# Kernel optimization log

Measured on AMD Instinct MI355X. Metric: run time of the kernel, lower is better.

Reference implementation:

```python
import jax, jax.numpy as jnp
import numpy as np

B, S, D = 2, 2048, 1024
H, HD = 16, 64          # n_heads, head_dim (H*HD == D)
E, K, F = 8, 2, 1024    # n_experts, top_k, expert hidden size
EPS = 1e-6


def setup_inputs() -> dict:
    key = jax.random.key(0)
    ks = jax.random.split(key, 10)
    g = lambda k, shape, sc: jax.random.normal(k, shape, jnp.float32) * sc
    return {
        "x": g(ks[0], (B, S, D), 1.0),
        "attn_norm_w": jnp.ones((D,), jnp.float32),
        "wq": g(ks[1], (D, D), 0.02),
        "wk": g(ks[2], (D, D), 0.02),
        "wv": g(ks[3], (D, D), 0.02),
        "wo": g(ks[4], (D, D), 0.02),
        "ffn_norm_w": jnp.ones((D,), jnp.float32),
        "router_w": g(ks[5], (D, E), 0.02),
        "w1": g(ks[6], (E, D, F), 0.02),  # gate proj per expert
        "w3": g(ks[7], (E, D, F), 0.02),  # up proj per expert
        "w2": g(ks[8], (E, F, D), 0.02),  # down proj per expert
    }


def rmsnorm(x, w):
    return x * jax.lax.rsqrt(jnp.mean(x * x, axis=-1, keepdims=True) + EPS) * w


def attention(x, wq, wk, wv, wo):
    b, s, d = x.shape
    q = (x @ wq).reshape(b, s, H, HD)
    k = (x @ wk).reshape(b, s, H, HD)
    v = (x @ wv).reshape(b, s, H, HD)
    scores = jnp.einsum("bqhd,bkhd->bhqk", q, k) / jnp.sqrt(jnp.float32(HD))
    causal = jnp.tril(jnp.ones((s, s), bool))
    scores = jnp.where(causal, scores, jnp.finfo(scores.dtype).min)
    p = jax.nn.softmax(scores, axis=-1)
    o = jnp.einsum("bhqk,bkhd->bqhd", p, v).reshape(b, s, d)
    return o @ wo


def moe_ffn(x, router_w, w1, w2, w3):
    b, s, d = x.shape
    xt = x.reshape(-1, d)                       # [T, D]
    probs = jax.nn.softmax(xt @ router_w, axis=-1)  # [T, E]
    gate, idx = jax.lax.top_k(probs, K)         # [T, K]
    gate = gate / jnp.sum(gate, axis=-1, keepdims=True)  # renormalize top-k
    T = xt.shape[0]
    combine = jnp.zeros((T, E), xt.dtype).at[jnp.arange(T)[:, None], idx].set(gate)
    out = jnp.zeros_like(xt)
    for e in range(E):  # fixed small loop over experts (dense-equivalent dispatch)
        h = jax.nn.silu(xt @ w1[e]) * (xt @ w3[e])
        out = out + combine[:, e:e + 1] * (h @ w2[e])
    return out.reshape(b, s, d)


def reference(x, attn_norm_w, wq, wk, wv, wo, ffn_norm_w, router_w, w1, w2, w3):
    # h = x + dropout(attn(norm(x)));  out = h + dropout(moe(norm(h)))  (dropout=0)
    h = x + attention(rmsnorm(x, attn_norm_w), wq, wk, wv, wo)
    return h + moe_ffn(rmsnorm(h, ffn_norm_w), router_w, w1, w2, w3)
```

## Files before the change

### kernel.cpp

```cpp
#include <hip/hip_runtime.h>
#include <cstdint>
#include <math.h>

typedef unsigned short u16;
typedef unsigned int u32;
typedef __bf16 bf16x8 __attribute__((ext_vector_type(8)));
typedef float f32x4 __attribute__((ext_vector_type(4)));

#define TBATCH 2
#define TSEQ   2048
#define TDIM   1024
#define THEADS 16
#define THDIM  64
#define TEXP   8
#define TFF    1024
#define TTOK   (TBATCH*TSEQ)
#define TPAIRS (TTOK*2)

__device__ __forceinline__ u16 f2bf(float f) {
  u32 u = __float_as_uint(f);
  u += 0x7FFFu + ((u >> 16) & 1u);
  return (u16)(u >> 16);
}
__device__ __forceinline__ u16 f2bft(float f) {
  return (u16)(__float_as_uint(f) >> 16);
}
__device__ __forceinline__ float bf2f(u16 h) { return __uint_as_float(((u32)h) << 16); }
__device__ __forceinline__ float fexp2(float x) {
  float r;
  asm("v_exp_f32 %0, %1" : "=v"(r) : "v"(x));
  return r;
}

__device__ __forceinline__ void gll16(const void* g, void* l) {
  __builtin_amdgcn_global_load_lds((const __attribute__((address_space(1))) void*)g,
                                   (__attribute__((address_space(3))) void*)l, 16, 0, 0);
}
__device__ __forceinline__ bf16x8 ldsread(const void* p) { return *(const bf16x8*)p; }
__device__ __forceinline__ f32x4 mm16(bf16x8 a, bf16x8 b, f32x4 c) {
  return __builtin_amdgcn_mfma_f32_16x16x32_bf16(a, b, c, 0, 0, 0);
}
__device__ __forceinline__ f32x4 fzero() { f32x4 z = {0.f, 0.f, 0.f, 0.f}; return z; }

__global__ void transpose_all_k(const float* __restrict__ wq, const float* __restrict__ wk,
                                const float* __restrict__ wv, const float* __restrict__ wo,
                                const float* __restrict__ w1, const float* __restrict__ w3,
                                const float* __restrict__ w2,
                                u16* __restrict__ qth, u16* __restrict__ qtl,
                                u16* __restrict__ kth, u16* __restrict__ ktl,
                                u16* __restrict__ vth_, u16* __restrict__ vtl_,
                                u16* __restrict__ oth, u16* __restrict__ otl,
                                u16* __restrict__ w1t, u16* __restrict__ w3t, u16* __restrict__ w2t) {
  __shared__ float t[32][33];
  int id = (int)blockIdx.x;
  const float* in; u16* outh; u16* outl = nullptr;
  size_t bo = 0;
  int tile;
  if (id < 4096) {
    const int wi = id >> 10;
    in   = (wi == 0) ? wq  : (wi == 1) ? wk  : (wi == 2) ? wv   : wo;
    outh = (wi == 0) ? qth : (wi == 1) ? kth : (wi == 2) ? vth_ : oth;
    outl = (wi == 0) ? qtl : (wi == 1) ? ktl : (wi == 2) ? vtl_ : otl;
    tile = id & 1023;
  } else {
    const int id2 = id - 4096;
    const int wi = id2 >> 13;
    const int rem = id2 & 8191;
    bo = (size_t)(rem >> 10) << 20;
    in   = (wi == 0) ? w1  : (wi == 1) ? w3  : w2;
    outh = (wi == 0) ? w1t : (wi == 1) ? w3t : w2t;
    tile = rem & 1023;
  }
  const int c0 = (tile & 31) * 32, r0 = (tile >> 5) * 32;
  const int tx = threadIdx.x, ty = threadIdx.y;
#pragma unroll
  for (int j = 0; j < 32; j += 8)
    t[ty + j][tx] = in[bo + (size_t)(r0 + ty + j) * 1024 + (c0 + tx)];
  __syncthreads();
#pragma unroll
  for (int j = 0; j < 32; j += 8) {
    float v = t[tx][ty + j];
    u16 hv = f2bf(v);
    size_t o = bo + (size_t)(c0 + ty + j) * 1024 + (r0 + tx);
    outh[o] = hv;
    if (outl != nullptr) outl[o] = f2bf(v - bf2f(hv));
  }
}

__launch_bounds__(256)
__global__ void rmsnorm_k(const float* __restrict__ x, const float* __restrict__ w,
                          u16* __restrict__ oh, u16* __restrict__ ol) {
  const int t = blockIdx.x, tid = threadIdx.x;
  const float4 xv = ((const float4*)(x + (size_t)t * TDIM))[tid];
  float ss = xv.x*xv.x + xv.y*xv.y + xv.z*xv.z + xv.w*xv.w;
#pragma unroll
  for (int d = 1; d < 64; d <<= 1) ss += __shfl_xor(ss, d, 64);
  __shared__ float sp[4];
  if ((tid & 63) == 0) sp[tid >> 6] = ss;
  __syncthreads();
  const float rsc = rsqrtf((sp[0] + sp[1] + sp[2] + sp[3]) * (1.0f / TDIM) + 1e-6f);
  const float4 wv = ((const float4*)w)[tid];
  float v0 = xv.x*rsc*wv.x, v1 = xv.y*rsc*wv.y, v2 = xv.z*rsc*wv.z, v3 = xv.w*rsc*wv.w;
  u16 h0 = f2bf(v0), h1 = f2bf(v1), h2 = f2bf(v2), h3 = f2bf(v3);
  uint2 ph; ph.x = (u32)h0 | ((u32)h1 << 16); ph.y = (u32)h2 | ((u32)h3 << 16);
  *(uint2*)(oh + (size_t)t * TDIM + tid * 4) = ph;
  u16 l0 = f2bf(v0 - bf2f(h0)), l1 = f2bf(v1 - bf2f(h1));
  u16 l2 = f2bf(v2 - bf2f(h2)), l3 = f2bf(v3 - bf2f(h3));
  uint2 pl; pl.x = (u32)l0 | ((u32)l1 << 16); pl.y = (u32)l2 | ((u32)l3 << 16);
  *(uint2*)(ol + (size_t)t * TDIM + tid * 4) = pl;
}

__launch_bounds__(256)
__global__ void gemm_qkv_k(const u16* __restrict__ Ah, const u16* __restrict__ Al,
                           const u16* __restrict__ Bqh, const u16* __restrict__ Bql,
                           const u16* __restrict__ Bkh, const u16* __restrict__ Bkl,
                           const u16* __restrict__ Bvh, const u16* __restrict__ Bvl,
                           u16* __restrict__ qh, u16* __restrict__ ql,
                           u16* __restrict__ kh, u16* __restrict__ kl,
                           u16* __restrict__ vth, u16* __restrict__ vtl) {
  __shared__ u16 sAh[2][128 * 32], sAl[2][128 * 32], sBh[2][64 * 32], sBl[2][64 * 32];
  const int tid = threadIdx.x, wid = tid >> 6, lane = tid & 63;
  const int which = blockIdx.y >> 4;
  const int m0 = blockIdx.x * 128, n0 = (blockIdx.y & 15) * 64;
  const int wr = wid >> 1, wc = wid & 1;
  const u16* Bth = (which == 0) ? Bqh : (which == 1) ? Bkh : Bvh;
  const u16* Btl = (which == 0) ? Bql : (which == 1) ? Bkl : Bvl;
  u16* outh = (which == 0) ? qh : kh;
  u16* outl = (which == 0) ? ql : kl;

  f32x4 acc[4][2];
#pragma unroll
  for (int i = 0; i < 4; i++)
#pragma unroll
    for (int j = 0; j < 2; j++) acc[i][j] = fzero();

  const int srow = tid >> 2;
  const int scol = (((tid & 3) ^ ((tid >> 3) & 3)) * 8);
  const size_t a0 = (size_t)(m0 + srow) * TDIM + scol;
  const size_t a1 = (size_t)(m0 + srow + 64) * TDIM + scol;
  const size_t b0 = (size_t)(n0 + srow) * TDIM + scol;
  const int ldsw = wid * 1024;

  const int g = (lane >> 1) & 3;
  int aoffs[4], boffs[2];
#pragma unroll
  for (int mf = 0; mf < 4; mf++)
    aoffs[mf] = (wr*64 + mf*16 + (lane & 15)) * 64 + ((((lane >> 4)) ^ g) << 4);
#pragma unroll
  for (int nf = 0; nf < 2; nf++)
    boffs[nf] = (wc*32 + nf*16 + (lane & 15)) * 64 + ((((lane >> 4)) ^ g) << 4);

  auto stage = [&](int kk, int bi) {
    const int ke = kk * 32;
    gll16(Ah + a0 + ke, (char*)sAh[bi] + ldsw);
    gll16(Ah + a1 + ke, (char*)sAh[bi] + 4096 + ldsw);
    gll16(Al + a0 + ke, (char*)sAl[bi] + ldsw);
    gll16(Al + a1 + ke, (char*)sAl[bi] + 4096 + ldsw);
    gll16(Bth + b0 + ke, (char*)sBh[bi] + ldsw);
    gll16(Btl + b0 + ke, (char*)sBl[bi] + ldsw);
  };

  stage(0, 0);
  asm volatile("s_waitcnt vmcnt(0)" ::: "memory");
  __builtin_amdgcn_s_barrier();

  for (int kk = 0; kk < 32; ++kk) {
    const int cur = kk & 1;
    if (kk + 1 < 32) stage(kk + 1, cur ^ 1);
    bf16x8 fah[4], fal[4], fbh[2], fbl[2];
#pragma unroll
    for (int mf = 0; mf < 4; mf++) { fah[mf] = ldsread((char*)sAh[cur] + aoffs[mf]); fal[mf] = ldsread((char*)sAl[cur] + aoffs[mf]); }
#pragma unroll
    for (int nf = 0; nf < 2; nf++) { fbh[nf] = ldsread((char*)sBh[cur] + boffs[nf]); fbl[nf] = ldsread((char*)sBl[cur] + boffs[nf]); }
#pragma unroll
    for (int mf = 0; mf < 4; mf++)
#pragma unroll
      for (int nf = 0; nf < 2; nf++) {
        acc[mf][nf] = mm16(fah[mf], fbh[nf], acc[mf][nf]);
        acc[mf][nf] = mm16(fah[mf], fbl[nf], acc[mf][nf]);
        acc[mf][nf] = mm16(fal[mf], fbh[nf], acc[mf][nf]);
      }
    asm volatile("s_waitcnt vmcnt(0)" ::: "memory");
    __builtin_amdgcn_s_barrier();
  }

#pragma unroll
  for (int mf = 0; mf < 4; mf++)
#pragma unroll
    for (int nf = 0; nf < 2; nf++)
#pragma unroll
      for (int r = 0; r < 4; r++) {
        const int grow = m0 + wr*64 + mf*16 + ((lane >> 4) * 4) + r;
        const int gcol = n0 + wc*32 + nf*16 + (lane & 15);
        const float v = acc[mf][nf][r];
        u16 hv = f2bf(v);
        u16 lv = f2bf(v - bf2f(hv));
        if (which < 2) {
          const size_t o = (size_t)grow * TDIM + gcol;
          outh[o] = hv; outl[o] = lv;
        } else {
          const int b = grow >> 11, s = grow & (TSEQ - 1);
          const int hh = gcol >> 6, hd = gcol & 63;
          const size_t o = ((size_t)((b * THEADS + hh) * THDIM + hd)) * TSEQ + s;
          vth[o] = hv; vtl[o] = lv;
        }
      }
}

template<int EPI>
__launch_bounds__(256)
__global__ void gemm_x3_k(const u16* __restrict__ Ah, const u16* __restrict__ Al,
                          const u16* __restrict__ Bth, const u16* __restrict__ Btl,
                          u16* __restrict__ outh, u16* __restrict__ outl,
                          float* __restrict__ outf, const float* __restrict__ resid,
                          int M, int N, int K) {
  __shared__ u16 sAh[2][128 * 32], sAl[2][128 * 32], sBh[2][64 * 32], sBl[2][64 * 32];
  const int tid = threadIdx.x, wid = tid >> 6, lane = tid & 63;
  const int m0 = blockIdx.x * 128, n0 = blockIdx.y * 64;
  const int wr = wid >> 1, wc = wid & 1;

  f32x4 acc[4][2];
#pragma unroll
  for (int i = 0; i < 4; i++)
#pragma unroll
    for (int j = 0; j < 2; j++) acc[i][j] = fzero();

  const int srow = tid >> 2;
  const int scol = (((tid & 3) ^ ((tid >> 3) & 3)) * 8);
  const size_t a0 = (size_t)(m0 + srow) * K + scol;
  const size_t a1 = (size_t)(m0 + srow + 64) * K + scol;
  const size_t b0 = (size_t)(n0 + srow) * K + scol;
  const int ldsw = wid * 1024;

  const int g = (lane >> 1) & 3;
  int aoffs[4], boffs[2];
#pragma unroll
  for (int mf = 0; mf < 4; mf++)
    aoffs[mf] = (wr*64 + mf*16 + (lane & 15)) * 64 + ((((lane >> 4)) ^ g) << 4);
#pragma unroll
  for (int nf = 0; nf < 2; nf++)
    boffs[nf] = (wc*32 + nf*16 + (lane & 15)) * 64 + ((((lane >> 4)) ^ g) << 4);

  auto stage = [&](int kk, int bi) {
    const int ke = kk * 32;
    gll16(Ah + a0 + ke, (char*)sAh[bi] + ldsw);
    gll16(Ah + a1 + ke, (char*)sAh[bi] + 4096 + ldsw);
    gll16(Al + a0 + ke, (char*)sAl[bi] + ldsw);
    gll16(Al + a1 + ke, (char*)sAl[bi] + 4096 + ldsw);
    gll16(Bth + b0 + ke, (char*)sBh[bi] + ldsw);
    gll16(Btl + b0 + ke, (char*)sBl[bi] + ldsw);
  };

  const int nk = K >> 5;
  stage(0, 0);
  asm volatile("s_waitcnt vmcnt(0)" ::: "memory");
  __builtin_amdgcn_s_barrier();

  for (int kk = 0; kk < nk; ++kk) {
    const int cur = kk & 1;
    if (kk + 1 < nk) stage(kk + 1, cur ^ 1);
    bf16x8 fah[4], fal[4], fbh[2], fbl[2];
#pragma unroll
    for (int mf = 0; mf < 4; mf++) { fah[mf] = ldsread((char*)sAh[cur] + aoffs[mf]); fal[mf] = ldsread((char*)sAl[cur] + aoffs[mf]); }
#pragma unroll
    for (int nf = 0; nf < 2; nf++) { fbh[nf] = ldsread((char*)sBh[cur] + boffs[nf]); fbl[nf] = ldsread((char*)sBl[cur] + boffs[nf]); }
#pragma unroll
    for (int mf = 0; mf < 4; mf++)
#pragma unroll
      for (int nf = 0; nf < 2; nf++) {
        acc[mf][nf] = mm16(fah[mf], fbh[nf], acc[mf][nf]);
        acc[mf][nf] = mm16(fah[mf], fbl[nf], acc[mf][nf]);
        acc[mf][nf] = mm16(fal[mf], fbh[nf], acc[mf][nf]);
      }
    asm volatile("s_waitcnt vmcnt(0)" ::: "memory");
    __builtin_amdgcn_s_barrier();
  }

#pragma unroll
  for (int mf = 0; mf < 4; mf++)
#pragma unroll
    for (int nf = 0; nf < 2; nf++)
#pragma unroll
      for (int r = 0; r < 4; r++) {
        const int grow = m0 + wr*64 + mf*16 + ((lane >> 4) * 4) + r;
        const int gcol = n0 + wc*32 + nf*16 + (lane & 15);
        const float v = acc[mf][nf][r];
        if (EPI == 0) {
          const size_t o = (size_t)grow * N + gcol;
          u16 hv = f2bf(v);
          outh[o] = hv; outl[o] = f2bf(v - bf2f(hv));
        } else if (EPI == 1) {
          const int b = grow >> 11, s = grow & (TSEQ - 1);
          const int hh = gcol >> 6, hd = gcol & 63;
          const size_t o = ((size_t)((b * THEADS + hh) * THDIM + hd)) * TSEQ + s;
          u16 hv = f2bf(v);
          outh[o] = hv; outl[o] = f2bf(v - bf2f(hv));
        } else {
          const size_t o = (size_t)grow * N + gcol;
          outf[o] = v + resid[o];
        }
      }
}

__launch_bounds__(256)
__global__ void flash_k(const u16* __restrict__ Qh, const u16* __restrict__ Ql,
                        const u16* __restrict__ Kh, const u16* __restrict__ Kl,
                        const u16* __restrict__ Vth, const u16* __restrict__ Vtl,
                        u16* __restrict__ Oh, u16* __restrict__ Ol) {
  __shared__ u16 sK[2][2][4096];
  __shared__ u16 sV[2][2][4096];
  __shared__ u16 sP[2][4][1024];
  const int tid = threadIdx.x, wid = tid >> 6, lane = tid & 63;
  const int qb = (int)(gridDim.x - 1 - blockIdx.x);
  const int bh = blockIdx.y;
  const int b = bh >> 4, h = bh & 15;
  const int srow = tid >> 3;
  const int sxcol = (((lane & 7) ^ ((lane >> 3) & 7)) << 3);
  const int ldsw = wid * 1024;
  const float SCL = 0.125f * 1.4426950408889634f;

  bf16x8 fqh[2][2], fql[2][2];
#pragma unroll
  for (int hh = 0; hh < 2; hh++) {
    const size_t qbase = ((size_t)(b * TSEQ + qb * 128 + hh * 64 + wid * 16 + (lane & 15))) * TDIM + h * 64;
#pragma unroll
    for (int kq = 0; kq < 2; kq++) {
      fqh[hh][kq] = *(const bf16x8*)(Qh + qbase + (kq * 4 + (lane >> 4)) * 8);
      fql[hh][kq] = *(const bf16x8*)(Ql + qbase + (kq * 4 + (lane >> 4)) * 8);
    }
  }

  f32x4 oacc[2][4];
  float m_run[2][4], l_lane[2][4];
#pragma unroll
  for (int hh = 0; hh < 2; hh++)
#pragma unroll
    for (int i = 0; i < 4; i++) { oacc[hh][i] = fzero(); m_run[hh][i] = -INFINITY; l_lane[hh][i] = 0.f; }

  const size_t kg0 = ((size_t)(b * TSEQ + srow)) * TDIM + h * 64 + sxcol;
  const size_t kg1 = kg0 + (size_t)32 * TDIM;
  const size_t vg0 = ((size_t)((b * THEADS + h) * THDIM + srow)) * TSEQ + sxcol;
  const size_t vg1 = vg0 + (size_t)32 * TSEQ;

  auto stage = [&](int kb, int bi) {
    const size_t ko = (size_t)kb * 64 * TDIM;
    const size_t vo = (size_t)kb * 64;
    gll16(Kh + kg0 + ko, (char*)sK[bi][0] + ldsw);
    gll16(Kh + kg1 + ko, (char*)sK[bi][0] + 4096 + ldsw);
    gll16(Kl + kg0 + ko, (char*)sK[bi][1] + ldsw);
    gll16(Kl + kg1 + ko, (char*)sK[bi][1] + 4096 + ldsw);
    gll16(Vth + vg0 + vo, (char*)sV[bi][0] + ldsw);
    gll16(Vth + vg1 + vo, (char*)sV[bi][0] + 4096 + ldsw);
    gll16(Vtl + vg0 + vo, (char*)sV[bi][1] + ldsw);
    gll16(Vtl + vg1 + vo, (char*)sV[bi][1] + 4096 + ldsw);
  };

  const int nkb = 2 * qb + 2;
  stage(0, 0);
  asm volatile("s_waitcnt vmcnt(0)" ::: "memory");
  __builtin_amdgcn_s_barrier();

  for (int kb = 0; kb < nkb; ++kb) {
    const int cur = kb & 1;
    if (kb + 1 < nkb) stage(kb + 1, cur ^ 1);

    f32x4 sc[2][4];
#pragma unroll
    for (int nf = 0; nf < 4; nf++) {
      f32x4 s0 = fzero(), s1 = fzero();
      const int krow = nf * 16 + (lane & 15);
#pragma unroll
      for (int kq = 0; kq < 2; kq++) {
        const int off = krow * 128 + (((kq * 4 + (lane >> 4)) ^ (lane & 7)) << 4);
        bf16x8 kfh = ldsread((char*)sK[cur][0] + off);
        bf16x8 kfl = ldsread((char*)sK[cur][1] + off);
        s0 = mm16(fqh[0][kq], kfh, s0);
        s0 = mm16(fqh[0][kq], kfl, s0);
        s0 = mm16(fql[0][kq], kfh, s0);
        s1 = mm16(fqh[1][kq], kfh, s1);
        s1 = mm16(fqh[1][kq], kfl, s1);
        s1 = mm16(fql[1][kq], kfh, s1);
      }
      sc[0][nf] = s0; sc[1][nf] = s1;
    }

#pragma unroll
    for (int hh = 0; hh < 2; hh++) {
      if (kb * 64 > qb * 128 + hh * 64 + 63) continue;

      const int qg = qb * 128 + hh * 64 + wid * 16 + ((lane >> 4) * 4);
      float pm[4] = {-INFINITY, -INFINITY, -INFINITY, -INFINITY};
#pragma unroll
      for (int nf = 0; nf < 4; nf++) {
        const int kg = kb * 64 + nf * 16 + (lane & 15);
#pragma unroll
        for (int r = 0; r < 4; r++) {
          float v = sc[hh][nf][r] * SCL;
          if (kg > qg + r) v = -INFINITY;
          sc[hh][nf][r] = v;
          pm[r] = fmaxf(pm[r], v);
        }
      }
#pragma unroll
      for (int r = 0; r < 4; r++)
#pragma unroll
        for (int d = 1; d < 16; d <<= 1) pm[r] = fmaxf(pm[r], __shfl_xor(pm[r], d, 64));

      float mn[4], esc[4];
#pragma unroll
      for (int r = 0; r < 4; r++) {
        mn[r] = fmaxf(m_run[hh][r], pm[r]);
        esc[r] = fexp2(m_run[hh][r] - mn[r]);
        m_run[hh][r] = mn[r];
      }
      float ls[4] = {0.f, 0.f, 0.f, 0.f};
#pragma unroll
      for (int nf = 0; nf < 4; nf++)
#pragma unroll
        for (int r = 0; r < 4; r++) {
          float p = fexp2(sc[hh][nf][r] - mn[r]);
          sc[hh][nf][r] = p;
          ls[r] += p;
        }
#pragma unroll
      for (int r = 0; r < 4; r++) l_lane[hh][r] = l_lane[hh][r] * esc[r] + ls[r];
#pragma unroll
      for (int nf = 0; nf < 4; nf++)
#pragma unroll
        for (int r = 0; r < 4; r++) oacc[hh][nf][r] *= esc[r];

#pragma unroll
      for (int nf = 0; nf < 4; nf++)
#pragma unroll
        for (int r = 0; r < 4; r++) {
          float p = sc[hh][nf][r];
          u16 ph = f2bft(p);
          const int prow = (lane >> 4) * 4 + r;
          const int pbyte = (prow * 128 + (nf * 16 + (lane & 15)) * 2) ^ ((prow & 7) << 4);
          *(u16*)((char*)sP[0][wid] + pbyte) = ph;
          *(u16*)((char*)sP[1][wid] + pbyte) = f2bft(p - bf2f(ph));
        }

#pragma unroll
      for (int kq = 0; kq < 2; kq++) {
        const int prow = lane & 15;
        const int poff = prow * 128 + (((kq * 4 + (lane >> 4)) ^ (prow & 7)) << 4);
        bf16x8 pah = ldsread((char*)sP[0][wid] + poff);
        bf16x8 pal = ldsread((char*)sP[1][wid] + poff);
#pragma unroll
        for (int nf = 0; nf < 4; nf++) {
          const int vrow = nf * 16 + (lane & 15);
          const int voff = vrow * 128 + (((kq * 4 + (lane >> 4)) ^ (lane & 7)) << 4);
          bf16x8 vfh = ldsread((char*)sV[cur][0] + voff);
          bf16x8 vfl = ldsread((char*)sV[cur][1] + voff);
          oacc[hh][nf] = mm16(pah, vfh, oacc[hh][nf]);
          oacc[hh][nf] = mm16(pah, vfl, oacc[hh][nf]);
          oacc[hh][nf] = mm16(pal, vfh, oacc[hh][nf]);
        }
      }
    }
    asm volatile("s_waitcnt vmcnt(0)" ::: "memory");
    __builtin_amdgcn_s_barrier();
  }

#pragma unroll
  for (int hh = 0; hh < 2; hh++)
#pragma unroll
    for (int r = 0; r < 4; r++) {
      float lt = l_lane[hh][r];
#pragma unroll
      for (int d = 1; d < 16; d <<= 1) lt += __shfl_xor(lt, d, 64);
      const float inv = 1.0f / lt;
      const int t = b * TSEQ + qb * 128 + hh * 64 + wid * 16 + ((lane >> 4) * 4) + r;
#pragma unroll
      for (int nf = 0; nf < 4; nf++) {
        const float v = oacc[hh][nf][r] * inv;
        const size_t o = (size_t)t * TDIM + h * 64 + nf * 16 + (lane & 15);
        u16 hv = f2bft(v);
        Oh[o] = hv; Ol[o] = f2bft(v - bf2f(hv));
      }
    }
}

__launch_bounds__(256)
__global__ void router_k(const float* __restrict__ hres, const float* __restrict__ wn,
                         const float* __restrict__ rw, u16* __restrict__ hn,
                         int* __restrict__ idx01, float* __restrict__ gate01,
                         int* __restrict__ counts) {
  const int t = blockIdx.x, tid = threadIdx.x;
  const float4 xv = ((const float4*)(hres + (size_t)t * TDIM))[tid];
  float ss = xv.x*xv.x + xv.y*xv.y + xv.z*xv.z + xv.w*xv.w;
#pragma unroll
  for (int d = 1; d < 64; d <<= 1) ss += __shfl_xor(ss, d, 64);
  __shared__ float sp[4];
  __shared__ float sacc[4][8];
  if ((tid & 63) == 0) sp[tid >> 6] = ss;
  __syncthreads();
  const float rsc = rsqrtf((sp[0]+sp[1]+sp[2]+sp[3]) * (1.0f / TDIM) + 1e-6f);
  const float4 wv = ((const float4*)wn)[tid];
  const float x0 = xv.x*rsc*wv.x, x1 = xv.y*rsc*wv.y, x2 = xv.z*rsc*wv.z, x3 = xv.w*rsc*wv.w;
  {
    u16 h0 = f2bf(x0), h1 = f2bf(x1), h2 = f2bf(x2), h3 = f2bf(x3);
    uint2 ph; ph.x = (u32)h0 | ((u32)h1 << 16); ph.y = (u32)h2 | ((u32)h3 << 16);
    *(uint2*)(hn + (size_t)t * TDIM + tid * 4) = ph;
  }
  const float* rp = rw + (size_t)(tid * 4) * TEXP;
  float acc[8];
#pragma unroll
  for (int e = 0; e < 8; e++) acc[e] = x0*rp[e] + x1*rp[8+e] + x2*rp[16+e] + x3*rp[24+e];
#pragma unroll
  for (int e = 0; e < 8; e++)
#pragma unroll
    for (int d = 1; d < 64; d <<= 1) acc[e] += __shfl_xor(acc[e], d, 64);
  if ((tid & 63) == 0)
#pragma unroll
    for (int e = 0; e < 8; e++) sacc[tid >> 6][e] = acc[e];
  __syncthreads();
  if (tid == 0) {
    float lg[8];
#pragma unroll
    for (int e = 0; e < 8; e++) lg[e] = sacc[0][e] + sacc[1][e] + sacc[2][e] + sacc[3][e];
    int i1 = 0;
#pragma unroll
    for (int e = 1; e < 8; e++) if (lg[e] > lg[i1]) i1 = e;
    int i2 = (i1 == 0) ? 1 : 0;
#pragma unroll
    for (int e = 0; e < 8; e++) if (e != i1 && lg[e] > lg[i2]) i2 = e;
    const float g1 = 1.0f / (1.0f + __expf(lg[i2] - lg[i1]));
    idx01[t*2] = i1; idx01[t*2+1] = i2;
    gate01[t*2] = g1; gate01[t*2+1] = 1.0f - g1;
    atomicAdd(&counts[i1], 1);
    atomicAdd(&counts[i2], 1);
  }
}

__global__ void zero8_k(int* counts) { if (threadIdx.x < TEXP) counts[threadIdx.x] = 0; }

__global__ void offsets_k(const int* __restrict__ counts, int* __restrict__ cursor,
                          int* __restrict__ bm_e, int* __restrict__ bm_s0,
                          int* __restrict__ bm_end, int* __restrict__ n_active) {
  if (threadIdx.x != 0 || blockIdx.x != 0) return;
  int off = 0, nb = 0;
  for (int e = 0; e < TEXP; e++) {
    const int c = counts[e];
    cursor[e] = off;
    const int end = off + c;
    for (int mb = 0; mb * 128 < c; mb++) { bm_e[nb] = e; bm_s0[nb] = off + mb * 128; bm_end[nb] = end; nb++; }
    off = end;
  }
  *n_active = nb;
}

__global__ void scatter_k(const int* __restrict__ idx01, int* __restrict__ cursor,
                          int* __restrict__ slot_of, int* __restrict__ perm) {
  const int t = blockIdx.x * 256 + threadIdx.x;
  if (t >= TTOK) return;
#pragma unroll
  for (int k = 0; k < 2; k++) {
    const int e = idx01[t*2+k];
    const int slot = atomicAdd(&cursor[e], 1);
    slot_of[t*2+k] = slot;
    perm[slot] = t;
  }
}

__launch_bounds__(256)
__global__ void moe_gemm1_k(const u16* __restrict__ hn, const u16* __restrict__ w1t,
                            const u16* __restrict__ w3t, const int* __restrict__ perm,
                            const int* __restrict__ bm_e, const int* __restrict__ bm_s0,
                            const int* __restrict__ bm_end, const int* __restrict__ n_active,
                            u16* __restrict__ hbuf) {
  if ((int)blockIdx.x >= *n_active) return;
  __shared__ u16 sA[2][128 * 32], sB1[2][64 * 32], sB3[2][64 * 32];
  const int tid = threadIdx.x, wid = tid >> 6, lane = tid & 63;
  const int e = bm_e[blockIdx.x], slot0 = bm_s0[blockIdx.x], send = bm_end[blockIdx.x];
  const int n0 = blockIdx.y * 64;
  const int wr = wid >> 1, wc = wid & 1;
  const int srow = tid >> 2;
  const int scol = (((tid & 3) ^ ((tid >> 3) & 3)) * 8);
  const int sa0 = slot0 + srow, sa1 = slot0 + srow + 64;
  const int ta = (sa0 < send) ? perm[sa0] : 0;
  const int tb2 = (sa1 < send) ? perm[sa1] : 0;
  const size_t a0 = (size_t)ta * TDIM + scol;
  const size_t a1 = (size_t)tb2 * TDIM + scol;
  const size_t bb = (size_t)e * TDIM * TFF + (size_t)(n0 + srow) * TDIM + scol;
  const int ldsw = wid * 1024;
  f32x4 ac1[4][2], ac3[4][2];
#pragma unroll
  for (int i = 0; i < 4; i++)
#pragma unroll
    for (int j = 0; j < 2; j++) { ac1[i][j] = fzero(); ac3[i][j] = fzero(); }
  const int g = (lane >> 1) & 3;
  int aoffs[4], boffs[2];
#pragma unroll
  for (int mf = 0; mf < 4; mf++)
    aoffs[mf] = (wr*64 + mf*16 + (lane & 15)) * 64 + ((((lane >> 4)) ^ g) << 4);
#pragma unroll
  for (int nf = 0; nf < 2; nf++)
    boffs[nf] = (wc*32 + nf*16 + (lane & 15)) * 64 + ((((lane >> 4)) ^ g) << 4);

  auto stage = [&](int kk, int bi) {
    const int ke = kk * 32;
    gll16(hn + a0 + ke, (char*)sA[bi] + ldsw);
    gll16(hn + a1 + ke, (char*)sA[bi] + 4096 + ldsw);
    gll16(w1t + bb + ke, (char*)sB1[bi] + ldsw);
    gll16(w3t + bb + ke, (char*)sB3[bi] + ldsw);
  };

  stage(0, 0);
  asm volatile("s_waitcnt vmcnt(0)" ::: "memory");
  __builtin_amdgcn_s_barrier();

  for (int kk = 0; kk < 32; ++kk) {
    const int cur = kk & 1;
    if (kk + 1 < 32) stage(kk + 1, cur ^ 1);
    bf16x8 fa[4], f1[2], f3[2];
#pragma unroll
    for (int mf = 0; mf < 4; mf++) fa[mf] = ldsread((char*)sA[cur] + aoffs[mf]);
#pragma unroll
    for (int nf = 0; nf < 2; nf++) { f1[nf] = ldsread((char*)sB1[cur] + boffs[nf]); f3[nf] = ldsread((char*)sB3[cur] + boffs[nf]); }
#pragma unroll
    for (int mf = 0; mf < 4; mf++)
#pragma unroll
      for (int nf = 0; nf < 2; nf++) {
        ac1[mf][nf] = mm16(fa[mf], f1[nf], ac1[mf][nf]);
        ac3[mf][nf] = mm16(fa[mf], f3[nf], ac3[mf][nf]);
      }
    asm volatile("s_waitcnt vmcnt(0)" ::: "memory");
    __builtin_amdgcn_s_barrier();
  }

#pragma unroll
  for (int mf = 0; mf < 4; mf++)
#pragma unroll
    for (int nf = 0; nf < 2; nf++)
#pragma unroll
      for (int r = 0; r < 4; r++) {
        const int slot = slot0 + wr*64 + mf*16 + ((lane >> 4) * 4) + r;
        if (slot < send) {
          const int col = n0 + wc*32 + nf*16 + (lane & 15);
          const float z1 = ac1[mf][nf][r], z3 = ac3[mf][nf][r];
          const float hv = z1 / (1.0f + __expf(-z1)) * z3;
          hbuf[(size_t)slot * TFF + col] = f2bf(hv);
        }
      }
}

__launch_bounds__(256)
__global__ void moe_gemm2_k(const u16* __restrict__ hbuf, const u16* __restrict__ w2t,
                            const int* __restrict__ bm_e, const int* __restrict__ bm_s0,
                            const int* __restrict__ bm_end, const int* __restrict__ n_active,
                            u16* __restrict__ pout) {
  if ((int)blockIdx.x >= *n_active) return;
  __shared__ u16 sA[2][128 * 32], sB[2][64 * 32];
  const int tid = threadIdx.x, wid = tid >> 6, lane = tid & 63;
  const int e = bm_e[blockIdx.x], slot0 = bm_s0[blockIdx.x], send = bm_end[blockIdx.x];
  const int n0 = blockIdx.y * 64;
  const int wr = wid >> 1, wc = wid & 1;
  const int srow = tid >> 2;
  const int scol = (((tid & 3) ^ ((tid >> 3) & 3)) * 8);
  int sa0 = slot0 + srow; if (sa0 > TPAIRS - 1) sa0 = TPAIRS - 1;
  int sa1 = slot0 + srow + 64; if (sa1 > TPAIRS - 1) sa1 = TPAIRS - 1;
  const size_t a0 = (size_t)sa0 * TFF + scol;
  const size_t a1 = (size_t)sa1 * TFF + scol;
  const size_t bb = (size_t)e * TDIM * TFF + (size_t)(n0 + srow) * TFF + scol;
  const int ldsw = wid * 1024;
  f32x4 acc[4][2];
#pragma unroll
  for (int i = 0; i < 4; i++)
#pragma unroll
    for (int j = 0; j < 2; j++) acc[i][j] = fzero();
  const int g = (lane >> 1) & 3;
  int aoffs[4], boffs[2];
#pragma unroll
  for (int mf = 0; mf < 4; mf++)
    aoffs[mf] = (wr*64 + mf*16 + (lane & 15)) * 64 + ((((lane >> 4)) ^ g) << 4);
#pragma unroll
  for (int nf = 0; nf < 2; nf++)
    boffs[nf] = (wc*32 + nf*16 + (lane & 15)) * 64 + ((((lane >> 4)) ^ g) << 4);

  auto stage = [&](int kk, int bi) {
    const int ke = kk * 32;
    gll16(hbuf + a0 + ke, (char*)sA[bi] + ldsw);
    gll16(hbuf + a1 + ke, (char*)sA[bi] + 4096 + ldsw);
    gll16(w2t + bb + ke, (char*)sB[bi] + ldsw);
  };

  stage(0, 0);
  asm volatile("s_waitcnt vmcnt(0)" ::: "memory");
  __builtin_amdgcn_s_barrier();

  for (int kk = 0; kk < 32; ++kk) {
    const int cur = kk & 1;
    if (kk + 1 < 32) stage(kk + 1, cur ^ 1);
    bf16x8 fa[4], fb[2];
#pragma unroll
    for (int mf = 0; mf < 4; mf++) fa[mf] = ldsread((char*)sA[cur] + aoffs[mf]);
#pragma unroll
    for (int nf = 0; nf < 2; nf++) fb[nf] = ldsread((char*)sB[cur] + boffs[nf]);
#pragma unroll
    for (int mf = 0; mf < 4; mf++)
#pragma unroll
      for (int nf = 0; nf < 2; nf++)
        acc[mf][nf] = mm16(fa[mf], fb[nf], acc[mf][nf]);
    asm volatile("s_waitcnt vmcnt(0)" ::: "memory");
    __builtin_amdgcn_s_barrier();
  }

#pragma unroll
  for (int mf = 0; mf < 4; mf++)
#pragma unroll
    for (int nf = 0; nf < 2; nf++)
#pragma unroll
      for (int r = 0; r < 4; r++) {
        const int slot = slot0 + wr*64 + mf*16 + ((lane >> 4) * 4) + r;
        if (slot < send) {
          const int col = n0 + wc*32 + nf*16 + (lane & 15);
          pout[(size_t)slot * TDIM + col] = f2bf(acc[mf][nf][r]);
        }
      }
}

__launch_bounds__(256)
__global__ void combine_k(const float* __restrict__ hres, const u16* __restrict__ pout,
                          const int* __restrict__ slot_of, const float* __restrict__ gate01,
                          float* __restrict__ out) {
  const int t = blockIdx.x, tid = threadIdx.x;
  const int s0 = slot_of[t*2], s1 = slot_of[t*2+1];
  const float g0 = gate01[t*2], g1 = gate01[t*2+1];
  const float4 hv = ((const float4*)(hres + (size_t)t * TDIM))[tid];
  const uint2 u0 = *(const uint2*)(pout + (size_t)s0 * TDIM + tid * 4);
  const uint2 u1 = *(const uint2*)(pout + (size_t)s1 * TDIM + tid * 4);
  float4 o;
  o.x = hv.x + g0 * bf2f((u16)(u0.x & 0xffff)) + g1 * bf2f((u16)(u1.x & 0xffff));
  o.y = hv.y + g0 * bf2f((u16)(u0.x >> 16))    + g1 * bf2f((u16)(u1.x >> 16));
  o.z = hv.z + g0 * bf2f((u16)(u0.y & 0xffff)) + g1 * bf2f((u16)(u1.y & 0xffff));
  o.w = hv.w + g0 * bf2f((u16)(u0.y >> 16))    + g1 * bf2f((u16)(u1.y >> 16));
  ((float4*)(out + (size_t)t * TDIM))[tid] = o;
}

extern "C" void kernel_launch(void* const* d_in, const int* in_sizes, int n_in,
                              void* d_out, int out_size, void* d_ws, size_t ws_size,
                              hipStream_t stream) {
  (void)in_sizes; (void)n_in; (void)out_size; (void)ws_size;
  const float* x   = (const float*)d_in[0];
  const float* anw = (const float*)d_in[1];
  const float* wq  = (const float*)d_in[2];
  const float* wk  = (const float*)d_in[3];
  const float* wv  = (const float*)d_in[4];
  const float* wo  = (const float*)d_in[5];
  const float* fnw = (const float*)d_in[6];
  const float* rw  = (const float*)d_in[7];
  const float* w1  = (const float*)d_in[8];
  const float* w3  = (const float*)d_in[9];
  const float* w2  = (const float*)d_in[10];
  float* out = (float*)d_out;

  char* ws = (char*)d_ws;
  size_t off = 0;
  auto take = [&](size_t bytes) -> char* {
    char* p = ws + off;
    off += (bytes + 255) & ~(size_t)255;
    return p;
  };
  const size_t SZ_W = (size_t)TDIM * TDIM * sizeof(u16);
  const size_t SZ_T = (size_t)TTOK * TDIM * sizeof(u16);
  u16* wqt_h = (u16*)take(SZ_W); u16* wqt_l = (u16*)take(SZ_W);
  u16* wkt_h = (u16*)take(SZ_W); u16* wkt_l = (u16*)take(SZ_W);
  u16* wvt_h = (u16*)take(SZ_W); u16* wvt_l = (u16*)take(SZ_W);
  u16* wot_h = (u16*)take(SZ_W); u16* wot_l = (u16*)take(SZ_W);
  u16* w1t = (u16*)take((size_t)TEXP * TDIM * TFF * sizeof(u16));
  u16* w3t = (u16*)take((size_t)TEXP * TDIM * TFF * sizeof(u16));
  u16* w2t = (u16*)take((size_t)TEXP * TDIM * TFF * sizeof(u16));
  u16* xnh = (u16*)take(SZ_T); u16* xnl = (u16*)take(SZ_T);
  u16* qh  = (u16*)take(SZ_T); u16* ql  = (u16*)take(SZ_T);
  u16* kh  = (u16*)take(SZ_T); u16* kl  = (u16*)take(SZ_T);
  u16* vth = (u16*)take(SZ_T); u16* vtl = (u16*)take(SZ_T);
  float* hres = (float*)take((size_t)TTOK * TDIM * sizeof(float));
  int*   idx01  = (int*)take(TTOK * 2 * 4);
  float* gate01 = (float*)take(TTOK * 2 * 4);
  int*   slot_of = (int*)take(TTOK * 2 * 4);
  int*   perm    = (int*)take(TPAIRS * 4);
  int*   counts  = (int*)take(256);
  int*   cursor  = (int*)take(256);
  int*   bm_e    = (int*)take(96 * 4);
  int*   bm_s0   = (int*)take(96 * 4);
  int*   bm_end  = (int*)take(96 * 4);
  int*   n_act   = (int*)take(256);
  u16* oh = xnh; u16* ol = xnl;
  u16* hn = qh;
  u16* hbuf = kh;
  u16* pout = vth;

  transpose_all_k<<<28672, dim3(32, 8), 0, stream>>>(wq, wk, wv, wo, w1, w3, w2,
                                                     wqt_h, wqt_l, wkt_h, wkt_l, wvt_h, wvt_l,
                                                     wot_h, wot_l, w1t, w3t, w2t);
  zero8_k<<<1, 64, 0, stream>>>(counts);
  rmsnorm_k<<<TTOK, 256, 0, stream>>>(x, anw, xnh, xnl);
  gemm_qkv_k<<<dim3(TTOK/128, 48), 256, 0, stream>>>(xnh, xnl, wqt_h, wqt_l, wkt_h, wkt_l,
                                                     wvt_h, wvt_l, qh, ql, kh, kl, vth, vtl);
  flash_k<<<dim3(TSEQ/128, TBATCH*THEADS), 256, 0, stream>>>(qh, ql, kh, kl, vth, vtl, oh, ol);
  gemm_x3_k<2><<<dim3(TTOK/128, TDIM/64), 256, 0, stream>>>(oh, ol, wot_h, wot_l, nullptr, nullptr, hres, x, TTOK, TDIM, TDIM);
  router_k<<<TTOK, 256, 0, stream>>>(hres, fnw, rw, hn, idx01, gate01, counts);
  offsets_k<<<1, 1, 0, stream>>>(counts, cursor, bm_e, bm_s0, bm_end, n_act);
  scatter_k<<<TTOK/256, 256, 0, stream>>>(idx01, cursor, slot_of, perm);
  moe_gemm1_k<<<dim3(72, TFF/64), 256, 0, stream>>>(hn, w1t, w3t, perm, bm_e, bm_s0, bm_end, n_act, hbuf);
  moe_gemm2_k<<<dim3(72, TDIM/64), 256, 0, stream>>>(hbuf, w2t, bm_e, bm_s0, bm_end, n_act, pout);
  combine_k<<<TTOK, 256, 0, stream>>>(hres, pout, slot_of, gate01, out);
}
```

Baseline: 584.6 us.

## Halve flash attention KV tile to 32 keys and raise occupancy bound

The flash attention kernel now streams 32-key K/V tiles instead of 64, halving shared memory for K, V and P buffers and setting launch bounds to allow 4 blocks per CU. The PV product is restructured so V fragments are loaded once per tile and shared by both query halves, with a new LDS swizzle for the narrower rows. The aim is higher occupancy and finer causal-mask skipping. The cost is twice as many loop iterations, each with its own barrier and wait, and more register pressure from the bound.

```diff
diff --git a/kernel.cpp b/kernel.cpp
--- a/kernel.cpp
+++ b/kernel.cpp
@@ -302,21 +302,18 @@
       }
 }
 
-__launch_bounds__(256)
+__launch_bounds__(256, 4)
 __global__ void flash_k(const u16* __restrict__ Qh, const u16* __restrict__ Ql,
                         const u16* __restrict__ Kh, const u16* __restrict__ Kl,
                         const u16* __restrict__ Vth, const u16* __restrict__ Vtl,
                         u16* __restrict__ Oh, u16* __restrict__ Ol) {
-  __shared__ u16 sK[2][2][4096];
-  __shared__ u16 sV[2][2][4096];
-  __shared__ u16 sP[2][4][1024];
+  __shared__ u16 sK[2][2][2048];
+  __shared__ u16 sV[2][2][2048];
+  __shared__ u16 sP[2][4][512];
   const int tid = threadIdx.x, wid = tid >> 6, lane = tid & 63;
   const int qb = (int)(gridDim.x - 1 - blockIdx.x);
   const int bh = blockIdx.y;
   const int b = bh >> 4, h = bh & 15;
-  const int srow = tid >> 3;
-  const int sxcol = (((lane & 7) ^ ((lane >> 3) & 7)) << 3);
-  const int ldsw = wid * 1024;
   const float SCL = 0.125f * 1.4426950408889634f;
 
   bf16x8 fqh[2][2], fql[2][2];
@@ -337,25 +334,24 @@
 #pragma unroll
     for (int i = 0; i < 4; i++) { oacc[hh][i] = fzero(); m_run[hh][i] = -INFINITY; l_lane[hh][i] = 0.f; }
 
-  const size_t kg0 = ((size_t)(b * TSEQ + srow)) * TDIM + h * 64 + sxcol;
-  const size_t kg1 = kg0 + (size_t)32 * TDIM;
-  const size_t vg0 = ((size_t)((b * THEADS + h) * THDIM + srow)) * TSEQ + sxcol;
-  const size_t vg1 = vg0 + (size_t)32 * TSEQ;
+  const int ksrow = tid >> 3;
+  const int ksxcol = (((lane & 7) ^ ((lane >> 3) & 7)) << 3);
+  const size_t kg0 = ((size_t)(b * TSEQ + ksrow)) * TDIM + h * 64 + ksxcol;
+  const int vsrow = tid >> 2;
+  const int vsxcol = (((tid & 3) ^ ((tid >> 3) & 3)) << 3);
+  const size_t vg0 = ((size_t)((b * THEADS + h) * THDIM + vsrow)) * TSEQ + vsxcol;
 
   auto stage = [&](int kb, int bi) {
-    const size_t ko = (size_t)kb * 64 * TDIM;
-    const size_t vo = (size_t)kb * 64;
-    gll16(Kh + kg0 + ko, (char*)sK[bi][0] + ldsw);
-    gll16(Kh + kg1 + ko, (char*)sK[bi][0] + 4096 + ldsw);
-    gll16(Kl + kg0 + ko, (char*)sK[bi][1] + ldsw);
-    gll16(Kl + kg1 + ko, (char*)sK[bi][1] + 4096 + ldsw);
-    gll16(Vth + vg0 + vo, (char*)sV[bi][0] + ldsw);
-    gll16(Vth + vg1 + vo, (char*)sV[bi][0] + 4096 + ldsw);
-    gll16(Vtl + vg0 + vo, (char*)sV[bi][1] + ldsw);
-    gll16(Vtl + vg1 + vo, (char*)sV[bi][1] + 4096 + ldsw);
+    const size_t ko = (size_t)kb * 32 * TDIM;
+    const size_t vo = (size_t)kb * 32;
+    const int wofs = wid * 1024;
+    gll16(Kh + kg0 + ko, (char*)sK[bi][0] + wofs);
+    gll16(Kl + kg0 + ko, (char*)sK[bi][1] + wofs);
+    gll16(Vth + vg0 + vo, (char*)sV[bi][0] + wofs);
+    gll16(Vtl + vg0 + vo, (char*)sV[bi][1] + wofs);
   };
 
-  const int nkb = 2 * qb + 2;
+  const int nkb = 4 * qb + 4;
   stage(0, 0);
   asm volatile("s_waitcnt vmcnt(0)" ::: "memory");
   __builtin_amdgcn_s_barrier();
@@ -364,9 +360,11 @@
     const int cur = kb & 1;
     if (kb + 1 < nkb) stage(kb + 1, cur ^ 1);
 
-    f32x4 sc[2][4];
-#pragma unroll
-    for (int nf = 0; nf < 4; nf++) {
+    const bool act0 = (kb * 32 <= qb * 128 + 63);
+
+    f32x4 sc[2][2];
+#pragma unroll
+    for (int nf = 0; nf < 2; nf++) {
       f32x4 s0 = fzero(), s1 = fzero();
       const int krow = nf * 16 + (lane & 15);
 #pragma unroll
@@ -384,15 +382,16 @@
       sc[0][nf] = s0; sc[1][nf] = s1;
     }
 
+    bf16x8 pa_h[2], pa_l[2];
 #pragma unroll
     for (int hh = 0; hh < 2; hh++) {
-      if (kb * 64 > qb * 128 + hh * 64 + 63) continue;
+      if (hh == 0 && !act0) continue;
 
       const int qg = qb * 128 + hh * 64 + wid * 16 + ((lane >> 4) * 4);
       float pm[4] = {-INFINITY, -INFINITY, -INFINITY, -INFINITY};
 #pragma unroll
-      for (int nf = 0; nf < 4; nf++) {
-        const int kg = kb * 64 + nf * 16 + (lane & 15);
+      for (int nf = 0; nf < 2; nf++) {
+        const int kg = kb * 32 + nf * 16 + (lane & 15);
 #pragma unroll
         for (int r = 0; r < 4; r++) {
           float v = sc[hh][nf][r] * SCL;
@@ -415,7 +414,7 @@
       }
       float ls[4] = {0.f, 0.f, 0.f, 0.f};
 #pragma unroll
-      for (int nf = 0; nf < 4; nf++)
+      for (int nf = 0; nf < 2; nf++)
 #pragma unroll
         for (int r = 0; r < 4; r++) {
           float p = fexp2(sc[hh][nf][r] - mn[r]);
@@ -430,35 +429,41 @@
         for (int r = 0; r < 4; r++) oacc[hh][nf][r] *= esc[r];
 
 #pragma unroll
-      for (int nf = 0; nf < 4; nf++)
+      for (int nf = 0; nf < 2; nf++)
 #pragma unroll
         for (int r = 0; r < 4; r++) {
           float p = sc[hh][nf][r];
           u16 ph = f2bft(p);
           const int prow = (lane >> 4) * 4 + r;
-          const int pbyte = (prow * 128 + (nf * 16 + (lane & 15)) * 2) ^ ((prow & 7) << 4);
+          const int pbyte = (prow * 64 + (nf * 16 + (lane & 15)) * 2) ^ (((prow >> 1) & 3) << 4);
           *(u16*)((char*)sP[0][wid] + pbyte) = ph;
           *(u16*)((char*)sP[1][wid] + pbyte) = f2bft(p - bf2f(ph));
         }
 
-#pragma unroll
-      for (int kq = 0; kq < 2; kq++) {
+      {
         const int prow = lane & 15;
-        const int poff = prow * 128 + (((kq * 4 + (lane >> 4)) ^ (prow & 7)) << 4);
-        bf16x8 pah = ldsread((char*)sP[0][wid] + poff);
-        bf16x8 pal = ldsread((char*)sP[1][wid] + poff);
-#pragma unroll
-        for (int nf = 0; nf < 4; nf++) {
-          const int vrow = nf * 16 + (lane & 15);
-          const int voff = vrow * 128 + (((kq * 4 + (lane >> 4)) ^ (lane & 7)) << 4);
-          bf16x8 vfh = ldsread((char*)sV[cur][0] + voff);
-          bf16x8 vfl = ldsread((char*)sV[cur][1] + voff);
-          oacc[hh][nf] = mm16(pah, vfh, oacc[hh][nf]);
-          oacc[hh][nf] = mm16(pah, vfl, oacc[hh][nf]);
-          oacc[hh][nf] = mm16(pal, vfh, oacc[hh][nf]);
-        }
+        const int poff = (prow * 64 + ((lane >> 4) << 4)) ^ ((((prow >> 1) & 3)) << 4);
+        pa_h[hh] = ldsread((char*)sP[0][wid] + poff);
+        pa_l[hh] = ldsread((char*)sP[1][wid] + poff);
       }
     }
+
+#pragma unroll
+    for (int nf = 0; nf < 4; nf++) {
+      const int vrow = nf * 16 + (lane & 15);
+      const int voff = vrow * 64 + ((((lane >> 4) ^ ((lane >> 1) & 3)) & 3) << 4);
+      bf16x8 vfh = ldsread((char*)sV[cur][0] + voff);
+      bf16x8 vfl = ldsread((char*)sV[cur][1] + voff);
+      if (act0) {
+        oacc[0][nf] = mm16(pa_h[0], vfh, oacc[0][nf]);
+        oacc[0][nf] = mm16(pa_h[0], vfl, oacc[0][nf]);
+        oacc[0][nf] = mm16(pa_l[0], vfh, oacc[0][nf]);
+      }
+      oacc[1][nf] = mm16(pa_h[1], vfh, oacc[1][nf]);
+      oacc[1][nf] = mm16(pa_h[1], vfl, oacc[1][nf]);
+      oacc[1][nf] = mm16(pa_l[1], vfh, oacc[1][nf]);
+    }
+
     asm volatile("s_waitcnt vmcnt(0)" ::: "memory");
     __builtin_amdgcn_s_barrier();
   }
```

Result: slower. 768.8 us (+31.5%).

## Share V fragment LDS reads across both query halves and lazily rescale softmax

Applied to the files above, without the earlier changes.

The PV product loop moves out of the per-half loop. Each V fragment is read from LDS once and applied to both 64-row query halves; the P fragments for each half are held in registers first. The online-softmax rescale of the accumulator and running sum now runs only when some lane's running max would grow by more than 8 in log2 units. Otherwise the stale max is kept and the rescale multiplies are skipped. This halves the V LDS traffic and removes most rescale work, at the cost of more live registers and probabilities up to 2^8 before normalization.

```diff
diff --git a/kernel.cpp b/kernel.cpp
--- a/kernel.cpp
+++ b/kernel.cpp
@@ -364,6 +364,8 @@
     const int cur = kb & 1;
     if (kb + 1 < nkb) stage(kb + 1, cur ^ 1);
 
+    const bool act0 = (kb * 64 <= qb * 128 + 63);
+
     f32x4 sc[2][4];
 #pragma unroll
     for (int nf = 0; nf < 4; nf++) {
@@ -384,9 +386,10 @@
       sc[0][nf] = s0; sc[1][nf] = s1;
     }
 
+    bf16x8 pa_h[2][2], pa_l[2][2];
 #pragma unroll
     for (int hh = 0; hh < 2; hh++) {
-      if (kb * 64 > qb * 128 + hh * 64 + 63) continue;
+      if (hh == 0 && !act0) continue;
 
       const int qg = qb * 128 + hh * 64 + wid * 16 + ((lane >> 4) * 4);
       float pm[4] = {-INFINITY, -INFINITY, -INFINITY, -INFINITY};
@@ -406,28 +409,30 @@
 #pragma unroll
         for (int d = 1; d < 16; d <<= 1) pm[r] = fmaxf(pm[r], __shfl_xor(pm[r], d, 64));
 
-      float mn[4], esc[4];
-#pragma unroll
-      for (int r = 0; r < 4; r++) {
-        mn[r] = fmaxf(m_run[hh][r], pm[r]);
-        esc[r] = fexp2(m_run[hh][r] - mn[r]);
-        m_run[hh][r] = mn[r];
+      const float dm = fmaxf(fmaxf(pm[0] - m_run[hh][0], pm[1] - m_run[hh][1]),
+                             fmaxf(pm[2] - m_run[hh][2], pm[3] - m_run[hh][3]));
+      if (!__all(dm <= 8.0f)) {
+#pragma unroll
+        for (int r = 0; r < 4; r++) {
+          const float mn = fmaxf(m_run[hh][r], pm[r]);
+          const float esc = fexp2(m_run[hh][r] - mn);
+          m_run[hh][r] = mn;
+          l_lane[hh][r] *= esc;
+#pragma unroll
+          for (int nf = 0; nf < 4; nf++) oacc[hh][nf][r] *= esc;
+        }
       }
       float ls[4] = {0.f, 0.f, 0.f, 0.f};
 #pragma unroll
       for (int nf = 0; nf < 4; nf++)
 #pragma unroll
         for (int r = 0; r < 4; r++) {
-          float p = fexp2(sc[hh][nf][r] - mn[r]);
+          float p = fexp2(sc[hh][nf][r] - m_run[hh][r]);
           sc[hh][nf][r] = p;
           ls[r] += p;
         }
 #pragma unroll
-      for (int r = 0; r < 4; r++) l_lane[hh][r] = l_lane[hh][r] * esc[r] + ls[r];
-#pragma unroll
-      for (int nf = 0; nf < 4; nf++)
-#pragma unroll
-        for (int r = 0; r < 4; r++) oacc[hh][nf][r] *= esc[r];
+      for (int r = 0; r < 4; r++) l_lane[hh][r] += ls[r];
 
 #pragma unroll
       for (int nf = 0; nf < 4; nf++)
@@ -445,20 +450,29 @@
       for (int kq = 0; kq < 2; kq++) {
         const int prow = lane & 15;
         const int poff = prow * 128 + (((kq * 4 + (lane >> 4)) ^ (prow & 7)) << 4);
-        bf16x8 pah = ldsread((char*)sP[0][wid] + poff);
-        bf16x8 pal = ldsread((char*)sP[1][wid] + poff);
-#pragma unroll
-        for (int nf = 0; nf < 4; nf++) {
-          const int vrow = nf * 16 + (lane & 15);
-          const int voff = vrow * 128 + (((kq * 4 + (lane >> 4)) ^ (lane & 7)) << 4);
-          bf16x8 vfh = ldsread((char*)sV[cur][0] + voff);
-          bf16x8 vfl = ldsread((char*)sV[cur][1] + voff);
-          oacc[hh][nf] = mm16(pah, vfh, oacc[hh][nf]);
-          oacc[hh][nf] = mm16(pah, vfl, oacc[hh][nf]);
-          oacc[hh][nf] = mm16(pal, vfh, oacc[hh][nf]);
+        pa_h[hh][kq] = ldsread((char*)sP[0][wid] + poff);
+        pa_l[hh][kq] = ldsread((char*)sP[1][wid] + poff);
+      }
+    }
+
+#pragma unroll
+    for (int kq = 0; kq < 2; kq++)
+#pragma unroll
+      for (int nf = 0; nf < 4; nf++) {
+        const int vrow = nf * 16 + (lane & 15);
+        const int voff = vrow * 128 + (((kq * 4 + (lane >> 4)) ^ (lane & 7)) << 4);
+        bf16x8 vfh = ldsread((char*)sV[cur][0] + voff);
+        bf16x8 vfl = ldsread((char*)sV[cur][1] + voff);
+        if (act0) {
+          oacc[0][nf] = mm16(pa_h[0][kq], vfh, oacc[0][nf]);
+          oacc[0][nf] = mm16(pa_h[0][kq], vfl, oacc[0][nf]);
+          oacc[0][nf] = mm16(pa_l[0][kq], vfh, oacc[0][nf]);
         }
-      }
-    }
+        oacc[1][nf] = mm16(pa_h[1][kq], vfh, oacc[1][nf]);
+        oacc[1][nf] = mm16(pa_h[1][kq], vfl, oacc[1][nf]);
+        oacc[1][nf] = mm16(pa_l[1][kq], vfh, oacc[1][nf]);
+      }
+
     asm volatile("s_waitcnt vmcnt(0)" ::: "memory");
     __builtin_amdgcn_s_barrier();
   }
```

Result: slower. 655.1 us (+12.1%).
